# Kernel optimization log

Measured on AMD Instinct MI355X. Metric: run time of the kernel, lower is better.

The kernel has to match this reference:

```python
import jax, jax.numpy as jnp
import numpy as np

E = 1024
B = 16384

def _ln(x, g, b, eps=1e-5):
    mu = jnp.mean(x, axis=-1, keepdims=True)
    var = jnp.mean(jnp.square(x - mu), axis=-1, keepdims=True)
    return (x - mu) * jax.lax.rsqrt(var + eps) * g + b

def setup_inputs() -> dict:
    key = jax.random.key(0)
    ks = jax.random.split(key, 16)
    s = 0.02
    return {
        'img_feat': jax.random.normal(ks[0], (B, E), jnp.float32),
        'txt_feat': jax.random.normal(ks[1], (B, E), jnp.float32),
        # MHA 1 (img queries txt): packed in_proj [3E, E] like torch
        'w_in1': jax.random.normal(ks[2], (3 * E, E), jnp.float32) * s,
        'b_in1': jnp.zeros((3 * E,), jnp.float32),
        'w_out1': jax.random.normal(ks[3], (E, E), jnp.float32) * s,
        'b_out1': jnp.zeros((E,), jnp.float32),
        # MHA 2 (txt queries img)
        'w_in2': jax.random.normal(ks[4], (3 * E, E), jnp.float32) * s,
        'b_in2': jnp.zeros((3 * E,), jnp.float32),
        'w_out2': jax.random.normal(ks[5], (E, E), jnp.float32) * s,
        'b_out2': jnp.zeros((E,), jnp.float32),
        # LayerNorms
        'g1': jnp.ones((E,), jnp.float32), 'be1': jnp.zeros((E,), jnp.float32),
        'g2': jnp.ones((E,), jnp.float32), 'be2': jnp.zeros((E,), jnp.float32),
        'g3': jnp.ones((E,), jnp.float32), 'be3': jnp.zeros((E,), jnp.float32),
        # FFN
        'w_ffn1': jax.random.normal(ks[6], (4 * E, E), jnp.float32) * s,
        'b_ffn1': jnp.zeros((4 * E,), jnp.float32),
        'w_ffn2': jax.random.normal(ks[7], (E, 4 * E), jnp.float32) * s,
        'b_ffn2': jnp.zeros((E,), jnp.float32),
    }

def _attn_seq1(q_in, kv_in, w_in, b_in, w_out, b_out):
    # seq_len==1 for both query and key: softmax over a single 1x1 score is
    # identically 1, so attention output == out_proj(v_proj(kv)). The q/k
    # projections cancel out exactly (same math as torch MHA in eval mode).
    wv = w_in[2 * E:]
    bv = b_in[2 * E:]
    v = kv_in @ wv.T + bv          # [B, E]
    return v @ w_out.T + b_out     # [B, E]

def reference(img_feat, txt_feat, w_in1, b_in1, w_out1, b_out1,
              w_in2, b_in2, w_out2, b_out2,
              g1, be1, g2, be2, g3, be3,
              w_ffn1, b_ffn1, w_ffn2, b_ffn2):
    img_att = _attn_seq1(img_feat, txt_feat, w_in1, b_in1, w_out1, b_out1)
    img = _ln(img_feat + img_att, g1, be1)
    txt_att = _attn_seq1(txt_feat, img, w_in2, b_in2, w_out2, b_out2)
    txt = _ln(txt_feat + txt_att, g2, be2)
    combined = img + txt
    h = jax.nn.gelu(combined @ w_ffn1.T + b_ffn1, approximate=False)
    ffn = h @ w_ffn2.T + b_ffn2
    return _ln(combined + ffn, g3, be3)
```

## Files before the change

### kernel.cpp

```cpp
#include <hip/hip_runtime.h>
#include <hip/hip_bf16.h>

typedef __bf16 bf16_t;
typedef __bf16 bf16x8 __attribute__((ext_vector_type(8)));
typedef __bf16 bf16x4 __attribute__((ext_vector_type(4)));
typedef float f32x4 __attribute__((ext_vector_type(4)));

static constexpr int E = 1024;
static constexpr int BROWS = 16384;
static constexpr size_t MB = 1ull << 20;

__device__ __forceinline__ float gelu_f(float x) {
  float t = __expf(-x * fmaf(0.0713548163f, x * x, 1.5957691216f));
  return x / (1.0f + t);
}

__global__ __launch_bounds__(256) void cvt_f32_bf16(const float* __restrict__ src,
                                                    bf16_t* __restrict__ dst, int n4) {
  int stride = gridDim.x * blockDim.x;
  for (int i = blockIdx.x * blockDim.x + threadIdx.x; i < n4; i += stride) {
    float4 v = reinterpret_cast<const float4*>(src)[i];
    bf16x4 o;
    o[0] = (bf16_t)v.x; o[1] = (bf16_t)v.y; o[2] = (bf16_t)v.z; o[3] = (bf16_t)v.w;
    reinterpret_cast<bf16x4*>(dst)[i] = o;
  }
}

__global__ __launch_bounds__(256) void cvt2_f32_bf16(const float* __restrict__ s1,
                                                     bf16_t* __restrict__ d1,
                                                     const float* __restrict__ s2,
                                                     bf16_t* __restrict__ d2, int n4) {
  int stride = gridDim.x * blockDim.x;
  for (int i = blockIdx.x * blockDim.x + threadIdx.x; i < 2 * n4; i += stride) {
    const float* src = (i < n4) ? s1 : s2;
    bf16_t* dst = (i < n4) ? d1 : d2;
    int k = (i < n4) ? i : i - n4;
    float4 v = reinterpret_cast<const float4*>(src)[k];
    bf16x4 o;
    o[0] = (bf16_t)v.x; o[1] = (bf16_t)v.y; o[2] = (bf16_t)v.z; o[3] = (bf16_t)v.w;
    reinterpret_cast<bf16x4*>(dst)[k] = o;
  }
}

__global__ __launch_bounds__(256) void cvt_transpose2(const float* __restrict__ in1,
                                                      bf16_t* __restrict__ out1,
                                                      const float* __restrict__ in2,
                                                      bf16_t* __restrict__ out2) {
  const float* in = blockIdx.z ? in2 : in1;
  bf16_t* out = blockIdx.z ? out2 : out1;
  __shared__ float t[64][65];
  const int bx = blockIdx.x * 64, by = blockIdx.y * 64;
  const int tid = threadIdx.x;
  const int r = tid >> 2, c4 = (tid & 3) * 16;
#pragma unroll
  for (int j = 0; j < 4; ++j) {
    float4 v = *reinterpret_cast<const float4*>(&in[(long)(by + r) * E + bx + c4 + j * 4]);
    t[r][c4 + j * 4 + 0] = v.x;
    t[r][c4 + j * 4 + 1] = v.y;
    t[r][c4 + j * 4 + 2] = v.z;
    t[r][c4 + j * 4 + 3] = v.w;
  }
  __syncthreads();
#pragma unroll
  for (int j = 0; j < 16; j += 4) {
    bf16x4 o;
    o[0] = (bf16_t)t[c4 + j + 0][r];
    o[1] = (bf16_t)t[c4 + j + 1][r];
    o[2] = (bf16_t)t[c4 + j + 2][r];
    o[3] = (bf16_t)t[c4 + j + 3][r];
    *reinterpret_cast<bf16x4*>(&out[(long)(bx + r) * E + by + c4 + j]) = o;
  }
}

__global__ __launch_bounds__(256) void fuse_bias2(const float* __restrict__ wo1,
                                                  const float* __restrict__ bv1,
                                                  const float* __restrict__ bo1,
                                                  float* __restrict__ out1,
                                                  const float* __restrict__ wo2,
                                                  const float* __restrict__ bv2,
                                                  const float* __restrict__ bo2,
                                                  float* __restrict__ out2) {
  const int gr = (blockIdx.x * 256 + threadIdx.x) >> 6;
  const int lane = threadIdx.x & 63;
  const int row = gr & 1023;
  const float* wo = (gr < 1024) ? wo1 : wo2;
  const float* bv = (gr < 1024) ? bv1 : bv2;
  const float* bo = (gr < 1024) ? bo1 : bo2;
  float* outb = (gr < 1024) ? out1 : out2;
  float s = 0.f;
  for (int k = lane; k < E; k += 64) s += wo[(long)row * E + k] * bv[k];
#pragma unroll
  for (int off = 32; off; off >>= 1) s += __shfl_down(s, off);
  if (lane == 0) outb[row] = s + bo[row];
}

__global__ __launch_bounds__(256) void gemm_small2(const bf16_t* __restrict__ A1,
                                                   const bf16_t* __restrict__ B1,
                                                   bf16_t* __restrict__ C1,
                                                   const bf16_t* __restrict__ A2,
                                                   const bf16_t* __restrict__ B2,
                                                   bf16_t* __restrict__ C2) {
  const int K = 1024, N = 1024;
  const int orig = blockIdx.x;
  const int wgid = (orig & 7) * 16 + (orig >> 3);
  const int bx = wgid & 7;
  const int byy = wgid >> 3;
  const bf16_t* A = (byy < 8) ? A1 : A2;
  const bf16_t* Bw = (byy < 8) ? B1 : B2;
  bf16_t* Cout = (byy < 8) ? C1 : C2;
  const int by = byy & 7;
  __shared__ bf16_t As[128 * 32];
  __shared__ bf16_t Bs[128 * 32];
  const int tid = threadIdx.x;
  const int lane = tid & 63;
  const int w = tid >> 6;
  const int wr = w >> 1, wc = w & 1;
  const long m0 = (long)by * 128;
  const long n0 = (long)bx * 128;
  const bf16_t* aSrc = A + (m0 + (tid >> 2)) * (long)K + (tid & 3) * 8;
  const bf16_t* bSrc = Bw + (n0 + (tid >> 2)) * (long)K + (tid & 3) * 8;
  f32x4 acc[4][4];
#pragma unroll
  for (int mi = 0; mi < 4; ++mi)
#pragma unroll
    for (int ni = 0; ni < 4; ++ni) acc[mi][ni] = {0.f, 0.f, 0.f, 0.f};
  const int nkt = K >> 5;
  for (int kt = 0; kt < nkt; ++kt) {
#pragma unroll
    for (int r = 0; r < 2; ++r) {
      __builtin_amdgcn_global_load_lds(
          (__attribute__((address_space(1))) void*)(aSrc + (long)r * 64 * K + kt * 32),
          (__attribute__((address_space(3))) void*)((char*)As + r * 4096 + w * 1024), 16, 0, 0);
      __builtin_amdgcn_global_load_lds(
          (__attribute__((address_space(1))) void*)(bSrc + (long)r * 64 * K + kt * 32),
          (__attribute__((address_space(3))) void*)((char*)Bs + r * 4096 + w * 1024), 16, 0, 0);
    }
    __syncthreads();
    bf16x8 af[4], bfv[4];
#pragma unroll
    for (int i = 0; i < 4; ++i) {
      af[i] = *reinterpret_cast<const bf16x8*>(
          &As[(wr * 64 + i * 16 + (lane & 15)) * 32 + (lane >> 4) * 8]);
      bfv[i] = *reinterpret_cast<const bf16x8*>(
          &Bs[(wc * 64 + i * 16 + (lane & 15)) * 32 + (lane >> 4) * 8]);
    }
#pragma unroll
    for (int mi = 0; mi < 4; ++mi)
#pragma unroll
      for (int ni = 0; ni < 4; ++ni)
        acc[mi][ni] = __builtin_amdgcn_mfma_f32_16x16x32_bf16(af[mi], bfv[ni], acc[mi][ni], 0, 0, 0);
    __syncthreads();
  }
  const long crow0 = m0 + wr * 64 + ((lane >> 4) * 4);
  const long ccol0 = n0 + wc * 64 + (lane & 15);
#pragma unroll
  for (int mi = 0; mi < 4; ++mi)
#pragma unroll
    for (int ni = 0; ni < 4; ++ni)
#pragma unroll
      for (int r = 0; r < 4; ++r)
        Cout[(crow0 + mi * 16 + r) * N + ccol0 + ni * 16] = (bf16_t)acc[mi][ni][r];
}

#define GLDS(gp, lp)                                                              \
  __builtin_amdgcn_global_load_lds((__attribute__((address_space(1))) void*)(gp), \
                                   (__attribute__((address_space(3))) void*)(lp), 16, 0, 0)

template <int ACT_GELU, int OUT_BF16>
__global__ __launch_bounds__(512, 4) void gemm128(const bf16_t* __restrict__ A,
                                                  const bf16_t* __restrict__ Bw,
                                                  const float* __restrict__ bias,
                                                  void* __restrict__ Cout, int K, int N,
                                                  int NBX) {
  __shared__ char smem[73728];
  const int nwg = gridDim.x;
  const int orig = blockIdx.x;
  const int q = nwg >> 3;
  const int wgid = (orig & 7) * q + (orig >> 3);
  const int bx = wgid % NBX;
  const int by = wgid / NBX;
  const long m0 = (long)by * 128;
  const long n0 = (long)bx * 256;

  const int tid = threadIdx.x;
  const int lane = tid & 63;
  const int w = tid >> 6;
  const int wr = w >> 2;
  const int wc = w & 3;

  const int sv = (lane & 7) ^ (lane >> 3);
  const int r2 = (lane >> 3) * 2 + (sv >> 2);
  const int kc = (sv & 3) * 8;
  const bf16_t* srcA = A + (m0 + w * 16 + r2) * (long)K + kc;
  const bf16_t* srcB0 = Bw + (n0 + w * 32 + r2) * (long)K + kc;
  const bf16_t* srcB1 = srcB0 + 16 * (long)K;

#define STAGE(s, t)                                    \
  {                                                    \
    char* sd = smem + (s) * 24576;                     \
    const long tt = (long)(t) * 32;                    \
    GLDS(srcA + tt, sd + w * 1024);                    \
    GLDS(srcB0 + tt, sd + 8192 + w * 2048);            \
    GLDS(srcB1 + tt, sd + 8192 + w * 2048 + 1024);     \
  }

  const int laneoff =
      ((lane >> 1) & 7) * 128 +
      ((((((lane & 1) << 2) | (lane >> 4))) ^ ((lane >> 1) & 7)) << 4);
  const int wrOff = wr * 4096;
  const int wcOff = wc * 4096;

  f32x4 acc[4][4];
#pragma unroll
  for (int mi = 0; mi < 4; ++mi)
#pragma unroll
    for (int ni = 0; ni < 4; ++ni) acc[mi][ni] = {0.f, 0.f, 0.f, 0.f};

  STAGE(0, 0);
  STAGE(1, 1);
  asm volatile("s_waitcnt vmcnt(3)" ::: "memory");
  asm volatile("s_barrier" ::: "memory");

  const int NS = K >> 5;
  int cur = 0;
#pragma unroll 1
  for (int j = 0; j < NS; ++j) {
    const char* sb = smem + cur * 24576;
    if (j + 2 < NS) {
      int nx = cur + 2;
      if (nx >= 3) nx -= 3;
      STAGE(nx, j + 2);
    }
    bf16x8 a[4], b[4];
#pragma unroll
    for (int i = 0; i < 4; ++i)
      a[i] = *reinterpret_cast<const bf16x8*>(sb + wrOff + i * 1024 + laneoff);
#pragma unroll
    for (int i = 0; i < 4; ++i)
      b[i] = *reinterpret_cast<const bf16x8*>(sb + 8192 + wcOff + i * 1024 + laneoff);
    __builtin_amdgcn_s_setprio(1);
#pragma unroll
    for (int mi = 0; mi < 4; ++mi)
#pragma unroll
      for (int ni = 0; ni < 4; ++ni)
        acc[mi][ni] = __builtin_amdgcn_mfma_f32_16x16x32_bf16(a[mi], b[ni], acc[mi][ni], 0, 0, 0);
    __builtin_amdgcn_s_setprio(0);
    if (j + 1 < NS) {
      asm volatile("s_waitcnt lgkmcnt(0)" ::: "memory");
      if (j + 2 < NS)
        asm volatile("s_waitcnt vmcnt(3)" ::: "memory");
      else
        asm volatile("s_waitcnt vmcnt(0)" ::: "memory");
      asm volatile("s_barrier" ::: "memory");
    }
    cur = (cur + 1 == 3) ? 0 : cur + 1;
  }

  float bv[4];
#pragma unroll
  for (int ni = 0; ni < 4; ++ni) bv[ni] = bias[n0 + wc * 64 + ni * 16 + (lane & 15)];
  const long crow0 = m0 + wr * 64 + ((lane >> 4) * 4);
  const long ccol0 = n0 + wc * 64 + (lane & 15);
#pragma unroll
  for (int mi = 0; mi < 4; ++mi) {
#pragma unroll
    for (int ni = 0; ni < 4; ++ni) {
#pragma unroll
      for (int rr = 0; rr < 4; ++rr) {
        float v = acc[mi][ni][rr] + bv[ni];
        if (ACT_GELU) v = gelu_f(v);
        long idx = (crow0 + mi * 16 + rr) * N + ccol0 + ni * 16;
        if (OUT_BF16)
          ((bf16_t*)Cout)[idx] = (bf16_t)v;
        else
          ((float*)Cout)[idx] = v;
      }
    }
  }
#undef STAGE
}
#undef GLDS

template <int MODE>
__global__ __launch_bounds__(256) void ln_k(const float* __restrict__ Xf,
                                            const bf16_t* __restrict__ Xb,
                                            const float* __restrict__ Yf,
                                            const bf16_t* __restrict__ Yb,
                                            const float* __restrict__ gamma,
                                            const float* __restrict__ beta,
                                            const bf16_t* __restrict__ addB,
                                            float* __restrict__ outF,
                                            bf16_t* __restrict__ outB) {
  const int tid = threadIdx.x;
  const long base = (long)blockIdx.x * E;
  float4 s;
  if (MODE < 2) {
    float4 xv = reinterpret_cast<const float4*>(Xf + base)[tid];
    bf16x4 yv = reinterpret_cast<const bf16x4*>(Yb + base)[tid];
    s.x = xv.x + (float)yv[0]; s.y = xv.y + (float)yv[1];
    s.z = xv.z + (float)yv[2]; s.w = xv.w + (float)yv[3];
  } else {
    bf16x4 xv = reinterpret_cast<const bf16x4*>(Xb + base)[tid];
    float4 yv = reinterpret_cast<const float4*>(Yf + base)[tid];
    s.x = (float)xv[0] + yv.x; s.y = (float)xv[1] + yv.y;
    s.z = (float)xv[2] + yv.z; s.w = (float)xv[3] + yv.w;
  }
  float sum = s.x + s.y + s.z + s.w;
  float sq = s.x * s.x + s.y * s.y + s.z * s.z + s.w * s.w;
#pragma unroll
  for (int off = 32; off > 0; off >>= 1) {
    sum += __shfl_down(sum, off);
    sq += __shfl_down(sq, off);
  }
  __shared__ float red[2][4];
  const int w = tid >> 6;
  if ((tid & 63) == 0) { red[0][w] = sum; red[1][w] = sq; }
  __syncthreads();
  float tot = red[0][0] + red[0][1] + red[0][2] + red[0][3];
  float tsq = red[1][0] + red[1][1] + red[1][2] + red[1][3];
  const float mu = tot * (1.0f / E);
  const float var = tsq * (1.0f / E) - mu * mu;
  const float rs = rsqrtf(var + 1e-5f);
  float4 gv = reinterpret_cast<const float4*>(gamma)[tid];
  float4 bvv = reinterpret_cast<const float4*>(beta)[tid];
  float4 o;
  o.x = (s.x - mu) * rs * gv.x + bvv.x;
  o.y = (s.y - mu) * rs * gv.y + bvv.y;
  o.z = (s.z - mu) * rs * gv.z + bvv.z;
  o.w = (s.w - mu) * rs * gv.w + bvv.w;
  if (MODE == 1) {
    bf16x4 av = reinterpret_cast<const bf16x4*>(addB + base)[tid];
    o.x += (float)av[0]; o.y += (float)av[1]; o.z += (float)av[2]; o.w += (float)av[3];
  }
  if (MODE == 2) {
    reinterpret_cast<float4*>(outF + base)[tid] = o;
  } else {
    bf16x4 ob;
    ob[0] = (bf16_t)o.x; ob[1] = (bf16_t)o.y; ob[2] = (bf16_t)o.z; ob[3] = (bf16_t)o.w;
    reinterpret_cast<bf16x4*>(outB + base)[tid] = ob;
  }
}

extern "C" void kernel_launch(void* const* d_in, const int* in_sizes, int n_in, void* d_out,
                              int out_size, void* d_ws, size_t ws_size, hipStream_t stream) {
  const float* img_feat = (const float*)d_in[0];
  const float* txt_feat = (const float*)d_in[1];
  const float* w_in1 = (const float*)d_in[2];
  const float* b_in1 = (const float*)d_in[3];
  const float* w_out1 = (const float*)d_in[4];
  const float* b_out1 = (const float*)d_in[5];
  const float* w_in2 = (const float*)d_in[6];
  const float* b_in2 = (const float*)d_in[7];
  const float* w_out2 = (const float*)d_in[8];
  const float* b_out2 = (const float*)d_in[9];
  const float* g1 = (const float*)d_in[10];
  const float* be1 = (const float*)d_in[11];
  const float* g2 = (const float*)d_in[12];
  const float* be2 = (const float*)d_in[13];
  const float* g3 = (const float*)d_in[14];
  const float* be3 = (const float*)d_in[15];
  const float* w_ffn1 = (const float*)d_in[16];
  const float* b_ffn1 = (const float*)d_in[17];
  const float* w_ffn2 = (const float*)d_in[18];
  const float* b_ffn2 = (const float*)d_in[19];

  if (ws_size < 184 * MB) return;
  char* ws = (char*)d_ws;
  bf16_t* TXTB = (bf16_t*)(ws + 0 * MB);
  bf16_t* ATT = (bf16_t*)(ws + 32 * MB);
  bf16_t* IMGB = (bf16_t*)(ws + 64 * MB);
  bf16_t* T0a = (bf16_t*)(ws + 64 * MB);
  bf16_t* T0b = (bf16_t*)(ws + 66 * MB);
  bf16_t* T1a = (bf16_t*)(ws + 68 * MB);
  bf16_t* T1b = (bf16_t*)(ws + 70 * MB);
  bf16_t* H = (bf16_t*)(ws + 0 * MB);
  bf16_t* COMB = (bf16_t*)(ws + 128 * MB);
  bf16_t* Wc1 = (bf16_t*)(ws + 160 * MB);
  bf16_t* Wc2 = (bf16_t*)(ws + 162 * MB);
  bf16_t* wf1b = (bf16_t*)(ws + 164 * MB);
  bf16_t* wf2b = (bf16_t*)(ws + 172 * MB);
  float* bias1 = (float*)d_out;
  float* bias2 = bias1 + E;

  dim3 blk(256);
  dim3 blk512(512);
  cvt_f32_bf16<<<dim3(2048), blk, 0, stream>>>(txt_feat, TXTB, BROWS * E / 4);
  cvt2_f32_bf16<<<dim3(2048), blk, 0, stream>>>(w_ffn1, wf1b, w_ffn2, wf2b, 4 * E * E / 4);

  cvt_transpose2<<<dim3(16, 16, 2), blk, 0, stream>>>(w_in1 + 2 * E * E, T0a,
                                                      w_in2 + 2 * E * E, T0b);
  cvt2_f32_bf16<<<dim3(1024), blk, 0, stream>>>(w_out1, T1a, w_out2, T1b, E * E / 4);
  gemm_small2<<<dim3(128), blk, 0, stream>>>(T1a, T0a, Wc1, T1b, T0b, Wc2);
  fuse_bias2<<<dim3(512), blk, 0, stream>>>(w_out1, b_in1 + 2 * E, b_out1, bias1,
                                            w_out2, b_in2 + 2 * E, b_out2, bias2);

  gemm128<0, 1><<<dim3(512), blk512, 0, stream>>>(TXTB, Wc1, bias1, ATT, E, E, 4);
  ln_k<0><<<dim3(BROWS), blk, 0, stream>>>(img_feat, nullptr, nullptr, ATT, g1, be1, nullptr,
                                           nullptr, IMGB);
  gemm128<0, 1><<<dim3(512), blk512, 0, stream>>>(IMGB, Wc2, bias2, ATT, E, E, 4);
  ln_k<1><<<dim3(BROWS), blk, 0, stream>>>(txt_feat, nullptr, nullptr, ATT, g2, be2, IMGB,
                                           nullptr, COMB);
  gemm128<1, 1><<<dim3(2048), blk512, 0, stream>>>(COMB, wf1b, b_ffn1, H, E, 4 * E, 16);
  gemm128<0, 0><<<dim3(512), blk512, 0, stream>>>(H, wf2b, b_ffn2, d_out, 4 * E, E, 4);
  ln_k<2><<<dim3(BROWS), blk, 0, stream>>>(nullptr, COMB, (float*)d_out, nullptr, g3, be3,
                                           nullptr, (float*)d_out, nullptr);
}
```

Before: 528.6 us.

## Replace 128x256 GEMM with 256x256 tile, K=64 double-buffered quadrant pipeline

Swaps the 128x256-tile GEMM, which used a three-stage 32-wide K pipeline, for a 256x256 tile. The new kernel uses 64-wide K steps, double-buffered LDS (128 KB) and a four-quadrant MFMA schedule that interleaves LDS reads and global-to-LDS prefetch with the compute phases. The larger tile doubles per-wave accumulator work and raises arithmetic intensity, which cuts global and LDS traffic per FLOP. In exchange it uses more registers and LDS, so occupancy drops to one workgroup per CU, and the grids halve, which can leave CUs idle for the N=1024 GEMMs (256 workgroups).

```diff
diff --git a/kernel.cpp b/kernel.cpp
--- a/kernel.cpp
+++ b/kernel.cpp
@@ -167,19 +167,19 @@
                                    (__attribute__((address_space(3))) void*)(lp), 16, 0, 0)
 
 template <int ACT_GELU, int OUT_BF16>
-__global__ __launch_bounds__(512, 4) void gemm128(const bf16_t* __restrict__ A,
-                                                  const bf16_t* __restrict__ Bw,
-                                                  const float* __restrict__ bias,
-                                                  void* __restrict__ Cout, int K, int N,
-                                                  int NBX) {
-  __shared__ char smem[73728];
+__global__ __launch_bounds__(512) void gemm256b(const bf16_t* __restrict__ A,
+                                                const bf16_t* __restrict__ Bw,
+                                                const float* __restrict__ bias,
+                                                void* __restrict__ Cout, int K, int N,
+                                                int NBX) {
+  __shared__ char smem[131072];
   const int nwg = gridDim.x;
   const int orig = blockIdx.x;
   const int q = nwg >> 3;
   const int wgid = (orig & 7) * q + (orig >> 3);
   const int bx = wgid % NBX;
   const int by = wgid / NBX;
-  const long m0 = (long)by * 128;
+  const long m0 = (long)by * 256;
   const long n0 = (long)bx * 256;
 
   const int tid = threadIdx.x;
@@ -188,81 +188,106 @@
   const int wr = w >> 2;
   const int wc = w & 3;
 
-  const int sv = (lane & 7) ^ (lane >> 3);
-  const int r2 = (lane >> 3) * 2 + (sv >> 2);
-  const int kc = (sv & 3) * 8;
-  const bf16_t* srcA = A + (m0 + w * 16 + r2) * (long)K + kc;
-  const bf16_t* srcB0 = Bw + (n0 + w * 32 + r2) * (long)K + kc;
-  const bf16_t* srcB1 = srcB0 + 16 * (long)K;
-
-#define STAGE(s, t)                                    \
-  {                                                    \
-    char* sd = smem + (s) * 24576;                     \
-    const long tt = (long)(t) * 32;                    \
-    GLDS(srcA + tt, sd + w * 1024);                    \
-    GLDS(srcB0 + tt, sd + 8192 + w * 2048);            \
-    GLDS(srcB1 + tt, sd + 8192 + w * 2048 + 1024);     \
-  }
-
-  const int laneoff =
-      ((lane >> 1) & 7) * 128 +
-      ((((((lane & 1) << 2) | (lane >> 4))) ^ ((lane >> 1) & 7)) << 4);
-  const int wrOff = wr * 4096;
-  const int wcOff = wc * 4096;
-
-  f32x4 acc[4][4];
-#pragma unroll
-  for (int mi = 0; mi < 4; ++mi)
+  const bf16_t* srcA = A + m0 * (long)K;
+  const bf16_t* srcB = Bw + n0 * (long)K;
+  const long koff = ((lane & 7) ^ (lane >> 3)) * 8;
+  const long srow = (long)(w * 8 + (lane >> 3));
+
+#define STAGE(SEL, h, t)                                                            \
+  {                                                                                 \
+    const bf16_t* _s = (SEL) ? srcB : srcA;                                         \
+    char* _d = smem + ((t)&1) * 65536 + (SEL)*32768 + (h)*16384 + w * 1024 + lane * 16; \
+    const long _r = (long)((h)*128) + srow;                                         \
+    GLDS(_s + _r * (long)K + (long)(t)*64 + koff, _d);                              \
+    GLDS(_s + (_r + 64) * (long)K + (long)(t)*64 + koff, _d + 8192);                \
+  }
+
+  const int xr = lane & 7;
+  const int o16 = lane >> 4;
+  const int sA0 = ((o16) ^ xr) << 4;
+  const int sA1 = ((4 + o16) ^ xr) << 4;
+  const int l15 = lane & 15;
+  const int aRow = l15 * 128;
+  const int bHalf = 32768 + (wc >> 1) * 16384;
+  const int bRow = ((wc & 1) * 64 + l15) * 128;
+
+#define RD_A(dst, db, qm)                                                              \
+  _Pragma("unroll") for (int mi = 0; mi < 4; ++mi) {                                   \
+    dst[mi * 2 + 0] = *reinterpret_cast<const bf16x8*>(                                \
+        smem + (db) + wr * 16384 + (qm)*8192 + mi * 2048 + aRow + sA0);                \
+    dst[mi * 2 + 1] = *reinterpret_cast<const bf16x8*>(                                \
+        smem + (db) + wr * 16384 + (qm)*8192 + mi * 2048 + aRow + sA1);                \
+  }
+#define RD_B(dst, db, qn)                                                              \
+  _Pragma("unroll") for (int nj = 0; nj < 2; ++nj) {                                   \
+    dst[nj * 2 + 0] = *reinterpret_cast<const bf16x8*>(                                \
+        smem + (db) + bHalf + (qn)*4096 + nj * 2048 + bRow + sA0);                     \
+    dst[nj * 2 + 1] = *reinterpret_cast<const bf16x8*>(                                \
+        smem + (db) + bHalf + (qn)*4096 + nj * 2048 + bRow + sA1);                     \
+  }
+#define MM(QM, QN, AR, BR)                                                             \
+  __builtin_amdgcn_s_setprio(1);                                                       \
+  _Pragma("unroll") for (int mi = 0; mi < 4; ++mi)                                     \
+      _Pragma("unroll") for (int nj = 0; nj < 2; ++nj)                                 \
+          _Pragma("unroll") for (int kk = 0; kk < 2; ++kk)                             \
+              acc[(QM)*4 + mi][(QN)*2 + nj] = __builtin_amdgcn_mfma_f32_16x16x32_bf16( \
+                  AR[mi * 2 + kk], BR[nj * 2 + kk], acc[(QM)*4 + mi][(QN)*2 + nj], 0, 0, 0); \
+  __builtin_amdgcn_s_setprio(0);
+#define BAR asm volatile("s_barrier" ::: "memory")
+#define LGKM0                                          \
+  asm volatile("s_waitcnt lgkmcnt(0)" ::: "memory");   \
+  __builtin_amdgcn_sched_barrier(0)
+
+  f32x4 acc[8][4];
+#pragma unroll
+  for (int mi = 0; mi < 8; ++mi)
 #pragma unroll
     for (int ni = 0; ni < 4; ++ni) acc[mi][ni] = {0.f, 0.f, 0.f, 0.f};
 
-  STAGE(0, 0);
-  STAGE(1, 1);
-  asm volatile("s_waitcnt vmcnt(3)" ::: "memory");
-  asm volatile("s_barrier" ::: "memory");
-
-  const int NS = K >> 5;
-  int cur = 0;
+  const int NT = K >> 6;
+  STAGE(0, 0, 0); STAGE(0, 1, 0); STAGE(1, 0, 0); STAGE(1, 1, 0);
+  STAGE(0, 0, 1); STAGE(0, 1, 1);
+  asm volatile("s_waitcnt vmcnt(4)" ::: "memory");
+  BAR;
+
+  bf16x8 aE[8], aO[8], bE[4], bO[4];
 #pragma unroll 1
-  for (int j = 0; j < NS; ++j) {
-    const char* sb = smem + cur * 24576;
-    if (j + 2 < NS) {
-      int nx = cur + 2;
-      if (nx >= 3) nx -= 3;
-      STAGE(nx, j + 2);
+  for (int t = 0; t < NT; ++t) {
+    const int db = (t & 1) * 65536;
+    RD_A(aE, db, 0);
+    RD_B(bE, db, 0);
+    if (t + 1 < NT) { STAGE(1, 0, t + 1); STAGE(1, 1, t + 1); }
+    BAR; LGKM0;
+    MM(0, 0, aE, bE);
+    BAR;
+    RD_B(bO, db, 1);
+    BAR; LGKM0;
+    MM(0, 1, aE, bO);
+    BAR;
+    RD_A(aO, db, 1);
+    BAR; LGKM0;
+    MM(1, 1, aO, bO);
+    BAR;
+    RD_B(bE, db, 0);
+    if (t + 2 < NT) {
+      STAGE(0, 0, t + 2);
+      STAGE(0, 1, t + 2);
+      asm volatile("s_waitcnt vmcnt(4)" ::: "memory");
+    } else {
+      asm volatile("s_waitcnt vmcnt(0)" ::: "memory");
     }
-    bf16x8 a[4], b[4];
-#pragma unroll
-    for (int i = 0; i < 4; ++i)
-      a[i] = *reinterpret_cast<const bf16x8*>(sb + wrOff + i * 1024 + laneoff);
-#pragma unroll
-    for (int i = 0; i < 4; ++i)
-      b[i] = *reinterpret_cast<const bf16x8*>(sb + 8192 + wcOff + i * 1024 + laneoff);
-    __builtin_amdgcn_s_setprio(1);
-#pragma unroll
-    for (int mi = 0; mi < 4; ++mi)
-#pragma unroll
-      for (int ni = 0; ni < 4; ++ni)
-        acc[mi][ni] = __builtin_amdgcn_mfma_f32_16x16x32_bf16(a[mi], b[ni], acc[mi][ni], 0, 0, 0);
-    __builtin_amdgcn_s_setprio(0);
-    if (j + 1 < NS) {
-      asm volatile("s_waitcnt lgkmcnt(0)" ::: "memory");
-      if (j + 2 < NS)
-        asm volatile("s_waitcnt vmcnt(3)" ::: "memory");
-      else
-        asm volatile("s_waitcnt vmcnt(0)" ::: "memory");
-      asm volatile("s_barrier" ::: "memory");
-    }
-    cur = (cur + 1 == 3) ? 0 : cur + 1;
+    BAR; LGKM0;
+    MM(1, 0, aO, bE);
+    BAR;
   }
 
   float bv[4];
 #pragma unroll
   for (int ni = 0; ni < 4; ++ni) bv[ni] = bias[n0 + wc * 64 + ni * 16 + (lane & 15)];
-  const long crow0 = m0 + wr * 64 + ((lane >> 4) * 4);
+  const long crow0 = m0 + wr * 128 + ((lane >> 4) * 4);
   const long ccol0 = n0 + wc * 64 + (lane & 15);
 #pragma unroll
-  for (int mi = 0; mi < 4; ++mi) {
+  for (int mi = 0; mi < 8; ++mi) {
 #pragma unroll
     for (int ni = 0; ni < 4; ++ni) {
 #pragma unroll
@@ -278,6 +303,11 @@
     }
   }
 #undef STAGE
+#undef RD_A
+#undef RD_B
+#undef MM
+#undef BAR
+#undef LGKM0
 }
 #undef GLDS
 
@@ -394,14 +424,14 @@
   fuse_bias2<<<dim3(512), blk, 0, stream>>>(w_out1, b_in1 + 2 * E, b_out1, bias1,
                                             w_out2, b_in2 + 2 * E, b_out2, bias2);
 
-  gemm128<0, 1><<<dim3(512), blk512, 0, stream>>>(TXTB, Wc1, bias1, ATT, E, E, 4);
+  gemm256b<0, 1><<<dim3(256), blk512, 0, stream>>>(TXTB, Wc1, bias1, ATT, E, E, 4);
   ln_k<0><<<dim3(BROWS), blk, 0, stream>>>(img_feat, nullptr, nullptr, ATT, g1, be1, nullptr,
                                            nullptr, IMGB);
-  gemm128<0, 1><<<dim3(512), blk512, 0, stream>>>(IMGB, Wc2, bias2, ATT, E, E, 4);
+  gemm256b<0, 1><<<dim3(256), blk512, 0, stream>>>(IMGB, Wc2, bias2, ATT, E, E, 4);
   ln_k<1><<<dim3(BROWS), blk, 0, stream>>>(txt_feat, nullptr, nullptr, ATT, g2, be2, IMGB,
                                            nullptr, COMB);
-  gemm128<1, 1><<<dim3(2048), blk512, 0, stream>>>(COMB, wf1b, b_ffn1, H, E, 4 * E, 16);
-  gemm128<0, 0><<<dim3(512), blk512, 0, stream>>>(H, wf2b, b_ffn2, d_out, 4 * E, E, 4);
+  gemm256b<1, 1><<<dim3(1024), blk512, 0, stream>>>(COMB, wf1b, b_ffn1, H, E, 4 * E, 16);
+  gemm256b<0, 0><<<dim3(256), blk512, 0, stream>>>(H, wf2b, b_ffn2, d_out, 4 * E, E, 4);
   ln_k<2><<<dim3(BROWS), blk, 0, stream>>>(nullptr, COMB, (float*)d_out, nullptr, g3, be3,
                                            nullptr, (float*)d_out, nullptr);
 }
```

After: 499.1 us, median of 2. 1.06x faster.
